# Performance work log

Measured on AMD Instinct MI355X. Metric: run time of the kernel, lower is better.

Reference implementation:

```python
import jax, jax.numpy as jnp
import numpy as np
from math import lgamma

LMAX = 4
SPHERE_FDIM = 512
SO3_F1 = 64
BATCH = 64
IMG = 509
EPS = 1e-5

# ---------- numpy setup-time Wigner / spherical-harmonic machinery ----------

def _lnf(n):
    return lgamma(n + 1.0)

def small_d(l, beta):
    # real Wigner small-d, rows m'=-l..l, cols m=-l..l, beta: (G,)
    G = beta.shape[0]
    d = np.zeros((G, 2*l+1, 2*l+1))
    cb, sb = np.cos(beta/2.0), np.sin(beta/2.0)
    for i, mp in enumerate(range(-l, l+1)):
        for j, m in enumerate(range(-l, l+1)):
            pref = 0.5*(_lnf(l+mp)+_lnf(l-mp)+_lnf(l+m)+_lnf(l-m))
            val = np.zeros(G)
            for k in range(max(0, m-mp), min(l+m, l-mp)+1):
                ln = pref - (_lnf(l+m-k)+_lnf(k)+_lnf(l-mp-k)+_lnf(mp-m+k))
                val += ((-1.0)**(mp-m+k))*np.exp(ln)*cb**(2*l+m-mp-2*k)*sb**(mp-m+2*k)
            d[:, i, j] = val
    return d

def _U(l):
    # complex->real spherical-harmonic change of basis
    U = np.zeros((2*l+1, 2*l+1), dtype=complex)
    U[l, l] = 1.0
    s = 2.0**-0.5
    for m in range(1, l+1):
        U[l+m, l+m] = ((-1)**m)*s
        U[l+m, l-m] = s
        U[l-m, l-m] = 1j*s
        U[l-m, l+m] = -1j*((-1)**m)*s
    return U

def wigner_D(l, a, b, c):
    # real-basis Wigner D, (G, 2l+1, 2l+1)
    d = small_d(l, b)
    m = np.arange(-l, l+1)
    Dc = np.exp(-1j*np.outer(a, m))[:, :, None]*d*np.exp(-1j*np.outer(c, m))[:, None, :]
    U = _U(l)
    return np.real(np.einsum('ij,gjk,lk->gil', U, Dc, U.conj()))

def flat_wigner(lmax, a, b, c):
    # (G, sum_l (2l+1)^2) with sqrt(2l+1) component normalization (orthonormal basis)
    return np.concatenate([np.sqrt(2*l+1.0)*wigner_D(l, a, b, c).reshape(len(a), -1) for l in range(lmax+1)], axis=1)

def sph_harm(lmax, alpha, beta):
    # component-normalized real spherical harmonics, (G, (lmax+1)^2)
    z = np.zeros_like(alpha)
    return np.concatenate([np.sqrt(2*l+1.0)*wigner_D(l, alpha, beta, z)[:, :, l] for l in range(lmax+1)], axis=1)

def fib_sphere(n):
    # quasi-uniform sphere grid (stand-in for healpix grid of same size)
    i = np.arange(n) + 0.5
    beta = np.arccos(1.0 - 2.0*i/n)
    alpha = (np.pi*(1.0+5.0**0.5)*i) % (2.0*np.pi)
    return alpha, beta

def so3_grid(n_s2, n_gamma):
    a, b = fib_sphere(n_s2)
    g = np.linspace(0, 2*np.pi, n_gamma, endpoint=False)
    return np.repeat(a, n_gamma), np.repeat(b, n_gamma), np.tile(g, n_s2)

# ---------- inputs ----------

def setup_inputs() -> dict:
    key = jax.random.key(0)
    ks = jax.random.split(key, 8)
    f32 = jnp.float32
    x = jax.random.normal(ks[0], (BATCH, 1, IMG, IMG), f32)
    conv1_w = jax.random.normal(ks[1], (3, 1, 5, 5), f32)*0.2
    conv1_b = jnp.zeros((3,), f32)
    conv2_w = jax.random.normal(ks[2], (5, 3, 5, 5), f32)*0.12
    conv2_b = jnp.zeros((5,), f32)
    p_w = jax.random.normal(ks[3], (SPHERE_FDIM, 5), f32)*0.4  # projector 1x1 conv
    p_b = jnp.zeros((SPHERE_FDIM,), f32)
    # projector: orthographic-projection gaussian weights onto upper-hemisphere grid
    a_p, b_p = fib_sphere(192)
    msk = b_p <= np.pi/2
    a_p, b_p = a_p[msk], b_p[msk]
    xyz = np.stack([np.sin(b_p)*np.cos(a_p), np.sin(b_p)*np.sin(a_p), np.cos(b_p)], 1)
    max_r = np.max(np.linalg.norm(xyz[:, [0, 2]], axis=1))
    sx, sy = 0.9*xyz[:, 2]/max_r, 0.9*xyz[:, 0]/max_r
    g = np.linspace(-1, 1, 125)
    gx, gy = np.meshgrid(g, g, indexing='ij')
    sig = 0.2
    data = np.exp(-((gx[..., None]-sx)**2 + (gy[..., None]-sy)**2)/(2*sig*sig))/np.sqrt(2*np.pi*sig*sig)
    data = data/data.sum((0, 1), keepdims=True)
    idx = np.arange(20)  # fixed n_subset=20 points (deterministic)
    proj_weight = jnp.asarray(data[:, :, idx], f32)          # (125,125,20) learned param
    Y_proj = jnp.asarray(sph_harm(LMAX, a_p[idx], b_p[idx]), f32)  # (20,25)
    # S2Convolution kernel grid: full sphere, 192 pts
    a_k, b_k = fib_sphere(192)
    Y_s2 = jnp.asarray(sph_harm(LMAX, a_k, b_k), f32)        # (192,25)
    s2_w = jax.random.normal(ks[4], (SPHERE_FDIM, SO3_F1, 192), f32)
    bn_gamma = jnp.ones((165,), f32)
    bn_beta = jnp.zeros((165,), f32)
    # SO3Convolution near-identity kernel grid (8 alpha x 3 beta x 8 gamma)
    beta_k = np.arange(1, 4)*(np.pi/8)/3
    alpha_k = np.linspace(0, 2*np.pi, 8, endpoint=False)
    gamma_k = np.linspace(0, 2*np.pi, 8, endpoint=False)
    A, B, C = np.meshgrid(alpha_k, beta_k, gamma_k, indexing='ij')
    D_so3k = jnp.asarray(flat_wigner(LMAX, A.ravel(), B.ravel(), C.ravel()), f32)  # (192,165)
    so3_w = jax.random.normal(ks[5], (SO3_F1, 1, A.size), f32)
    # SO3Activation grid (576 rotations) and evaluation grid (4608 rotations)
    D_act = jnp.asarray(flat_wigner(LMAX, *so3_grid(48, 12)), f32)             # (576,165)
    eval_wigners = jnp.asarray(flat_wigner(LMAX, *so3_grid(192, 24)).T, f32)   # (165,4608)
    return {"x": x, "conv1_w": conv1_w, "conv1_b": conv1_b, "conv2_w": conv2_w, "conv2_b": conv2_b, "p_w": p_w, "p_b": p_b, "proj_weight": proj_weight, "Y_proj": Y_proj, "s2_w": s2_w, "Y_s2": Y_s2, "bn_gamma": bn_gamma, "bn_beta": bn_beta, "so3_w": so3_w, "D_so3k": D_so3k, "D_act": D_act, "eval_wigners": eval_wigners}

# ---------- forward ----------

def _conv(x, w, b):
    y = jax.lax.conv_general_dilated(x, w, (2, 2), 'VALID', dimension_numbers=('NCHW', 'OIHW', 'NCHW'))
    return y + b[None, :, None, None]

def _forward(x, conv1_w, conv1_b, conv2_w, conv2_b, p_w, p_b, proj_weight, Y_proj, s2_w, Y_s2, bn_gamma, bn_beta, so3_w, D_so3k, D_act, eval_wigners):
    # CNN featurizer: (B,1,509,509) -> (B,5,125,125)
    feat = _conv(jax.nn.relu(_conv(x, conv1_w, conv1_b)), conv2_w, conv2_b)
    f0 = feat[0]  # original forward only uses sample 0
    # Image2Sphere projector: 1x1 conv, gaussian projection to sphere pts, SH expansion
    z = jnp.einsum('chw,oc->ohw', f0, p_w) + p_b[:, None, None]          # (512,125,125)
    pts = jnp.einsum('ohw,hwp->op', z, proj_weight)                       # (512,20)
    harm = jnp.einsum('op,pm->om', pts, Y_proj)/(Y_proj.shape[0]**0.5)    # (512,25)
    psi = jnp.einsum('ni,xyn->xyi', Y_s2, s2_w)/(Y_s2.shape[0]**0.5)      # (512,64,25)
    f_in = harm.shape[0]
    blocks, o = [], 0
    for l in range(LMAX+1):
        d = 2*l+1
        out_l = jnp.einsum('xyu,xm->yum', psi[:, :, o:o+d], harm[:, o:o+d])/(f_in**0.5)
        blocks.append(out_l.reshape(-1, d*d))
        o += d
    h = jnp.concatenate(blocks, axis=1)  # (64,165)
    # SO3Activation: to SO(3) grid, pointwise relu (normalize2mom factor sqrt(2)), back
    s = (2.0**0.5)*jax.nn.relu(jnp.einsum('fi,gi->fg', h, D_act))
    h = jnp.einsum('fg,gi->fi', s, D_act)/D_act.shape[0]
    # BatchNorm1d(165) over the 64-channel 'batch' dim, training statistics
    mu = h.mean(0)
    var = jnp.mean((h - mu)**2, axis=0)
    h = (h - mu)*jax.lax.rsqrt(var + EPS)*bn_gamma + bn_beta
    # SO3Convolution: so3 irreps -> so3 irreps, f_out=1
    psi2 = jnp.einsum('ni,xyn->xyi', D_so3k, so3_w)/(D_so3k.shape[0]**0.5)  # (64,1,165)
    blocks, o = [], 0
    for l in range(LMAX+1):
        d = 2*l+1
        pl = psi2[:, :, o:o+d*d].reshape(SO3_F1, -1, d, d)
        xl = h[:, o:o+d*d].reshape(SO3_F1, d, d)
        out_l = jnp.einsum('xyuv,xvm->yum', pl, xl)/((SO3_F1*d)**0.5)
        blocks.append(out_l.reshape(-1, d*d))
        o += d*d
    harm_out = jnp.concatenate(blocks, axis=1)  # (1,165)
    # probabilities over SO(3) grid: wigner matmul + sigmoid
    return jax.nn.sigmoid(jnp.matmul(harm_out, eval_wigners)).squeeze(0)  # (4608,)

def reference(x, conv1_w, conv1_b, conv2_w, conv2_b, p_w, p_b, proj_weight, Y_proj, s2_w, Y_s2, bn_gamma, bn_beta, so3_w, D_so3k, D_act, eval_wigners):
    return _forward(x, conv1_w, conv1_b, conv2_w, conv2_b, p_w, p_b, proj_weight, Y_proj, s2_w, Y_s2, bn_gamma, bn_beta, so3_w, D_so3k, D_act, eval_wigners)
```

## Files before the change

### kernel.cpp

```cpp
#include <hip/hip_runtime.h>
#include <math.h>

#define IMG 509
#define C1N 253
#define C2N 125
#define NSPH 512
#define NY 64
#define NK 192
#define NH 25
#define NI 165
#define NG 576
#define NE 4608
#define NP 20
#define YN 12288
#define PSPLIT 16

__device__ __forceinline__ void decode_irr(int t, int& l, int& o, int& d, int& u, int& m) {
    if (t < 1)       { l = 0; o = 0;  }
    else if (t < 10) { l = 1; o = 1;  }
    else if (t < 35) { l = 2; o = 10; }
    else if (t < 84) { l = 3; o = 35; }
    else             { l = 4; o = 84; }
    d = 2 * l + 1;
    int r = t - o;
    u = r / d;
    m = r - u * d;
}

__global__ __launch_bounds__(256) void k_conv(const float* __restrict__ x,
        const float* __restrict__ w1, const float* __restrict__ b1,
        const float* __restrict__ w2, const float* __restrict__ b2,
        float* __restrict__ f0) {
    __shared__ float s1[3][35][36];
    __shared__ float sw1[75];
    __shared__ float sw2[375];
    int tid = threadIdx.x;
    if (tid < 75) sw1[tid] = w1[tid];
    for (int j = tid; j < 375; j += 256) sw2[j] = w2[j];
    int OH0 = blockIdx.y * 16, OW0 = blockIdx.x * 16;
    int R0 = 2 * OH0, C0 = 2 * OW0;
    float bb0 = b1[0], bb1 = b1[1], bb2 = b1[2];
    __syncthreads();
    for (int j = tid; j < 35 * 35; j += 256) {
        int rr = j / 35, cc = j - rr * 35;
        int r = R0 + rr, c = C0 + cc;
        float v0 = 0.f, v1 = 0.f, v2 = 0.f;
        if (r < C1N && c < C1N) {
            const float* xp = x + (2 * r) * IMG + 2 * c;
            float a0 = bb0, a1 = bb1, a2 = bb2;
#pragma unroll
            for (int kh = 0; kh < 5; ++kh)
#pragma unroll
                for (int kw = 0; kw < 5; ++kw) {
                    float xv = xp[kh * IMG + kw];
                    a0 = fmaf(xv, sw1[kh * 5 + kw], a0);
                    a1 = fmaf(xv, sw1[25 + kh * 5 + kw], a1);
                    a2 = fmaf(xv, sw1[50 + kh * 5 + kw], a2);
                }
            v0 = fmaxf(a0, 0.f); v1 = fmaxf(a1, 0.f); v2 = fmaxf(a2, 0.f);
        }
        s1[0][rr][cc] = v0; s1[1][rr][cc] = v1; s1[2][rr][cc] = v2;
    }
    __syncthreads();
    int loh = tid >> 4, low = tid & 15;
    int oh = OH0 + loh, ow = OW0 + low;
    if (oh < C2N && ow < C2N) {
        float acc[5] = {b2[0], b2[1], b2[2], b2[3], b2[4]};
#pragma unroll
        for (int ci = 0; ci < 3; ++ci)
#pragma unroll
            for (int kh = 0; kh < 5; ++kh)
#pragma unroll
                for (int kw = 0; kw < 5; ++kw) {
                    float sv = s1[ci][2 * loh + kh][2 * low + kw];
                    int wof = ci * 25 + kh * 5 + kw;
#pragma unroll
                    for (int c = 0; c < 5; ++c)
                        acc[c] = fmaf(sv, sw2[c * 75 + wof], acc[c]);
                }
#pragma unroll
        for (int c = 0; c < 5; ++c)
            f0[c * (C2N * C2N) + oh * C2N + ow] = acc[c];
    }
}

__global__ __launch_bounds__(256) void k_proj(const float* __restrict__ f0,
        const float* __restrict__ proj, float* __restrict__ Gp) {
    int c = blockIdx.x, s = blockIdx.y, tid = threadIdx.x;
    const int HW = C2N * C2N;
    const int CH = (HW + PSPLIT - 1) / PSPLIT;
    int hw_end = min(HW, (s + 1) * CH);
    float acc[NP];
#pragma unroll
    for (int p = 0; p < NP; ++p) acc[p] = 0.0f;
    for (int hw = s * CH + tid; hw < hw_end; hw += 256) {
        float v = (c < 5) ? f0[c * HW + hw] : 1.0f;
        const float* pp = proj + (size_t)hw * NP;
#pragma unroll
        for (int p = 0; p < NP; ++p) acc[p] = fmaf(v, pp[p], acc[p]);
    }
    __shared__ float red[4][NP];
    int lane = tid & 63, wv = tid >> 6;
#pragma unroll
    for (int p = 0; p < NP; ++p) {
        float v = acc[p];
        for (int off = 32; off; off >>= 1) v += __shfl_xor(v, off, 64);
        if (lane == 0) red[wv][p] = v;
    }
    __syncthreads();
    if (tid < NP)
        Gp[(s * 6 + c) * NP + tid] = red[0][tid] + red[1][tid] + red[2][tid] + red[3][tid];
}

__global__ __launch_bounds__(256) void k_harm(const float* __restrict__ Gp,
        const float* __restrict__ p_w, const float* __restrict__ p_b,
        const float* __restrict__ Yp, float* __restrict__ harm) {
    __shared__ float sG[6 * NP];
    __shared__ float sY[NP * NH];
    int tid = threadIdx.x;
    if (tid < 6 * NP) {
        float a = 0.0f;
        for (int s = 0; s < PSPLIT; ++s) a += Gp[s * (6 * NP) + tid];
        sG[tid] = a;
    }
    for (int i = tid; i < NP * NH; i += 256) sY[i] = Yp[i];
    __syncthreads();
    int idx = blockIdx.x * 256 + tid;
    if (idx >= NSPH * NH) return;
    int o = idx / NH, m = idx - o * NH;
    float pb = p_b[o];
    const float* pw = p_w + o * 5;
    float acc = 0.0f;
#pragma unroll
    for (int p = 0; p < NP; ++p) {
        float pts = pb * sG[5 * NP + p];
#pragma unroll
        for (int cc = 0; cc < 5; ++cc) pts = fmaf(pw[cc], sG[cc * NP + p], pts);
        acc = fmaf(pts, sY[p * NH + m], acc);
    }
    harm[idx] = acc * (1.0f / 4.47213595499957939f);
}

#define XCH 64
__global__ __launch_bounds__(256) void k_T(const float* __restrict__ s2w,
        const float* __restrict__ harm, float* __restrict__ T, int atomic) {
    int yn = blockIdx.x * 256 + threadIdx.x;
    int x0 = blockIdx.y * XCH;
    __shared__ float sh[XCH * NH];
    for (int i = threadIdx.x; i < XCH * NH; i += 256) sh[i] = harm[x0 * NH + i];
    __syncthreads();
    float acc[NH];
#pragma unroll
    for (int m = 0; m < NH; ++m) acc[m] = 0.0f;
    const float* ap = s2w + (size_t)x0 * YN + yn;
#pragma unroll 8
    for (int xi = 0; xi < XCH; ++xi) {
        float a = ap[(size_t)xi * YN];
        const float* hr = sh + xi * NH;
#pragma unroll
        for (int m = 0; m < NH; ++m) acc[m] = fmaf(a, hr[m], acc[m]);
    }
    if (atomic) {
#pragma unroll
        for (int m = 0; m < NH; ++m) atomicAdd(T + (size_t)m * YN + yn, acc[m]);
    } else {
        float* tp = T + (size_t)(blockIdx.y * NH) * YN + yn;
#pragma unroll
        for (int m = 0; m < NH; ++m) tp[(size_t)m * YN] = acc[m];
    }
}

__global__ __launch_bounds__(576) void k_so3block(const float* __restrict__ T,
        const float* __restrict__ Ys2, const float* __restrict__ Dact,
        float* __restrict__ h2, int nparts) {
    int y = blockIdx.x, tid = threadIdx.x;
    __shared__ float sY[NK * NH];
    __shared__ float sT[NK * NH];
    __shared__ float shh[NI];
    __shared__ float ss[NG];
    for (int i = tid; i < NK * NH; i += NG) sY[i] = Ys2[i];
    for (int j = tid; j < NK * NH; j += NG) {
        int m = j / NK, n = j - m * NK;
        float acc = 0.0f;
        const float* tp = T + (size_t)m * YN + y * NK + n;
        for (int p = 0; p < nparts; ++p) acc += tp[(size_t)p * NH * YN];
        sT[n * NH + m] = acc;
    }
    __syncthreads();
    if (tid < NI) {
        int l, o, d, u, m;
        decode_irr(tid, l, o, d, u, m);
        int cu = l * l + u, cm = l * l + m;
        float acc = 0.0f;
        for (int n = 0; n < NK; ++n)
            acc = fmaf(sY[n * NH + cu], sT[n * NH + cm], acc);
        shh[tid] = acc * (1.0f / 313.534098402587976f);
    }
    __syncthreads();
    {
        const float* dr = Dact + (size_t)tid * NI;
        float acc = 0.0f;
        for (int i = 0; i < NI; ++i) acc = fmaf(shh[i], dr[i], acc);
        ss[tid] = 1.41421356237309515f * fmaxf(acc, 0.0f);
    }
    __syncthreads();
    if (tid < NI) {
        float acc = 0.0f;
        for (int g = 0; g < NG; ++g) acc = fmaf(ss[g], Dact[(size_t)g * NI + tid], acc);
        h2[y * NI + tid] = acc * (1.0f / (float)NG);
    }
}

__global__ __launch_bounds__(192) void k_psi2(const float* __restrict__ w,
        const float* __restrict__ D, float* __restrict__ psi2) {
    __shared__ float sw[NK];
    int x = blockIdx.x, t = threadIdx.x;
    if (t < NK) sw[t] = w[x * NK + t];
    __syncthreads();
    if (t >= NI) return;
    float acc = 0.0f;
    for (int n = 0; n < NK; ++n) acc = fmaf(sw[n], D[(size_t)n * NI + t], acc);
    psi2[x * NI + t] = acc * (1.0f / 13.8564064605510175f);
}

__global__ __launch_bounds__(192) void k_eval(const float* __restrict__ psi2,
        const float* __restrict__ h2, const float* __restrict__ gamma,
        const float* __restrict__ beta, const float* __restrict__ ew,
        float* __restrict__ out) {
    __shared__ float sp[NY * NI];
    __shared__ float sh[NY * NI];
    __shared__ float sho[NI];
    int tid = threadIdx.x;
    for (int i = tid; i < NY * NI; i += 192) { sp[i] = psi2[i]; sh[i] = h2[i]; }
    __syncthreads();
    if (tid < NI) {
        float s = 0.0f;
        for (int f = 0; f < NY; ++f) s += sh[f * NI + tid];
        float mu = s * (1.0f / NY);
        float v = 0.0f;
        for (int f = 0; f < NY; ++f) { float d = sh[f * NI + tid] - mu; v = fmaf(d, d, v); }
        float sc = rsqrtf(v * (1.0f / NY) + 1e-5f) * gamma[tid];
        float bt = beta[tid];
        for (int f = 0; f < NY; ++f) sh[f * NI + tid] = (sh[f * NI + tid] - mu) * sc + bt;
    }
    __syncthreads();
    if (tid < NI) {
        int l, o, d, u, m;
        decode_irr(tid, l, o, d, u, m);
        const float invsc[5] = {0.125f, 0.0721687836487032f, 0.0559016994374947f,
                                0.0472455591261534f, 0.0416666666666667f};
        float acc = 0.0f;
        for (int x = 0; x < NY; ++x) {
            const float* pr = sp + x * NI + o;
            const float* hr = sh + x * NI + o;
            for (int v = 0; v < d; ++v) acc = fmaf(pr[u * d + v], hr[v * d + m], acc);
        }
        sho[tid] = acc * invsc[l];
    }
    __syncthreads();
    if (tid < 96) {
        int g = blockIdx.x * 96 + tid;
        float acc = 0.0f;
        for (int i = 0; i < NI; ++i) acc = fmaf(sho[i], ew[(size_t)i * NE + g], acc);
        out[g] = 1.0f / (1.0f + expf(-acc));
    }
}

extern "C" void kernel_launch(void* const* d_in, const int* in_sizes, int n_in,
                              void* d_out, int out_size, void* d_ws, size_t ws_size,
                              hipStream_t stream) {
    const float* x      = (const float*)d_in[0];
    const float* c1w    = (const float*)d_in[1];
    const float* c1b    = (const float*)d_in[2];
    const float* c2w    = (const float*)d_in[3];
    const float* c2b    = (const float*)d_in[4];
    const float* p_w    = (const float*)d_in[5];
    const float* p_b    = (const float*)d_in[6];
    const float* projw  = (const float*)d_in[7];
    const float* Yp     = (const float*)d_in[8];
    const float* s2w    = (const float*)d_in[9];
    const float* Ys2    = (const float*)d_in[10];
    const float* gamma  = (const float*)d_in[11];
    const float* beta   = (const float*)d_in[12];
    const float* so3w   = (const float*)d_in[13];
    const float* Dso3k  = (const float*)d_in[14];
    const float* Dact   = (const float*)d_in[15];
    const float* ew     = (const float*)d_in[16];
    float* out = (float*)d_out;

    float* ws   = (float*)d_ws;
    float* f0   = ws;
    float* Gp   = f0 + 78128;
    float* harm = Gp + 1920;
    float* h2   = harm + 12800;
    float* psi2 = h2 + 10560;
    float* T    = psi2 + 10560;

    const size_t base = 78128 + 1920 + 12800 + 10560 + 10560;
    bool big = ws_size >= (base + 8u * 307200u) * sizeof(float);
    int nparts = big ? 8 : 1;
    if (!big) hipMemsetAsync(T, 0, (size_t)307200 * sizeof(float), stream);

    k_conv<<<dim3(8, 8), 256, 0, stream>>>(x, c1w, c1b, c2w, c2b, f0);
    k_proj<<<dim3(6, PSPLIT), 256, 0, stream>>>(f0, projw, Gp);
    k_harm<<<(NSPH * NH + 255) / 256, 256, 0, stream>>>(Gp, p_w, p_b, Yp, harm);
    k_T<<<dim3(48, 8), 256, 0, stream>>>(s2w, harm, T, big ? 0 : 1);
    k_so3block<<<NY, NG, 0, stream>>>(T, Ys2, Dact, h2, nparts);
    k_psi2<<<NY, 192, 0, stream>>>(so3w, Dso3k, psi2);
    k_eval<<<48, 192, 0, stream>>>(psi2, h2, gamma, beta, ew, out);
}
```

Baseline: 249.6 us.

## Fuse conv, projection, transpose and psi2 into one prologue kernel; refactor T stage

Merges the conv, projection, psi2, the T zeroing and a new Dact transpose into a single multi-role prologue kernel, so the pipeline runs as four launches instead of seven plus a memset. The conv is recomputed per output channel in row strips and fused directly with the projection reduction. The T stage now folds p_w/p_b in algebraically, accumulating 6 coefficients per s2w element instead of 25, and always uses atomics into a single T buffer. The final kernel splits the wigner dot over 4 wave-groups with 64 outputs per block, and so3block reads a transposed Dact for coalesced access. In exchange, the conv is redone once per output channel, and the T stage now always pays atomic contention where it previously could write per-part buffers when the workspace was large.

```diff
diff --git a/kernel.cpp b/kernel.cpp
--- a/kernel.cpp
+++ b/kernel.cpp
@@ -13,7 +13,6 @@
 #define NE 4608
 #define NP 20
 #define YN 12288
-#define PSPLIT 16
 
 __device__ __forceinline__ void decode_irr(int t, int& l, int& o, int& d, int& u, int& m) {
     if (t < 1)       { l = 0; o = 0;  }
@@ -27,152 +26,158 @@
     m = r - u * d;
 }
 
-__global__ __launch_bounds__(256) void k_conv(const float* __restrict__ x,
+__global__ __launch_bounds__(256) void k_pre(const float* __restrict__ x,
         const float* __restrict__ w1, const float* __restrict__ b1,
         const float* __restrict__ w2, const float* __restrict__ b2,
-        float* __restrict__ f0) {
-    __shared__ float s1[3][35][36];
+        const float* __restrict__ projw,
+        const float* __restrict__ Dact, float* __restrict__ DactT,
+        const float* __restrict__ so3w, const float* __restrict__ Dso3k,
+        float* __restrict__ psi2, float* __restrict__ Gp, float* __restrict__ T) {
+    __shared__ float s1[3 * 13 * 254];
     __shared__ float sw1[75];
-    __shared__ float sw2[375];
+    __shared__ float sw2[75];
+    __shared__ float red[4][NP];
+    int b = blockIdx.x, tid = threadIdx.x;
+    if (b < 150) {
+        int c = b / 25, s = b - 25 * c;
+        float acc[NP];
+#pragma unroll
+        for (int p = 0; p < NP; ++p) acc[p] = 0.0f;
+        if (c < 5) {
+            if (tid < 75) { sw1[tid] = w1[tid]; sw2[tid] = w2[c * 75 + tid]; }
+            __syncthreads();
+            float bb0 = b1[0], bb1 = b1[1], bb2 = b1[2];
+            for (int j = tid; j < 13 * 253; j += 256) {
+                int lq = j / 253, col = j - lq * 253;
+                int q = 10 * s + lq;
+                const float* xp = x + (2 * q) * IMG + 2 * col;
+                float a0 = bb0, a1 = bb1, a2 = bb2;
+#pragma unroll
+                for (int kh = 0; kh < 5; ++kh)
+#pragma unroll
+                    for (int kw = 0; kw < 5; ++kw) {
+                        float xv = xp[kh * IMG + kw];
+                        a0 = fmaf(xv, sw1[kh * 5 + kw], a0);
+                        a1 = fmaf(xv, sw1[25 + kh * 5 + kw], a1);
+                        a2 = fmaf(xv, sw1[50 + kh * 5 + kw], a2);
+                    }
+                s1[lq * 254 + col] = fmaxf(a0, 0.f);
+                s1[13 * 254 + lq * 254 + col] = fmaxf(a1, 0.f);
+                s1[2 * 13 * 254 + lq * 254 + col] = fmaxf(a2, 0.f);
+            }
+            __syncthreads();
+            float b2c = b2[c];
+            for (int j = tid; j < 625; j += 256) {
+                int lr = j / 125, ow = j - lr * 125;
+                float v = b2c;
+#pragma unroll
+                for (int ci = 0; ci < 3; ++ci)
+#pragma unroll
+                    for (int kh = 0; kh < 5; ++kh)
+#pragma unroll
+                        for (int kw = 0; kw < 5; ++kw)
+                            v = fmaf(s1[ci * (13 * 254) + (2 * lr + kh) * 254 + 2 * ow + kw],
+                                     sw2[ci * 25 + kh * 5 + kw], v);
+                const float* pp = projw + (size_t)(625 * s + j) * NP;
+#pragma unroll
+                for (int p = 0; p < NP; ++p) acc[p] = fmaf(v, pp[p], acc[p]);
+            }
+        } else {
+            for (int j = tid; j < 625; j += 256) {
+                const float* pp = projw + (size_t)(625 * s + j) * NP;
+#pragma unroll
+                for (int p = 0; p < NP; ++p) acc[p] += pp[p];
+            }
+        }
+        int lane = tid & 63, wv = tid >> 6;
+#pragma unroll
+        for (int p = 0; p < NP; ++p) {
+            float v = acc[p];
+            for (int off = 32; off; off >>= 1) v += __shfl_xor(v, off, 64);
+            if (lane == 0) red[wv][p] = v;
+        }
+        __syncthreads();
+        if (tid < NP)
+            Gp[(s * 6 + c) * NP + tid] = red[0][tid] + red[1][tid] + red[2][tid] + red[3][tid];
+    } else if (b < 522) {
+        int j = (b - 150) * 256 + tid;
+        if (j < NG * NI) {
+            int g = j / NI, i = j - g * NI;
+            DactT[(size_t)i * NG + g] = Dact[j];
+        }
+    } else if (b < 586) {
+        __shared__ float sw[NK];
+        int xx = b - 522;
+        if (tid < NK) sw[tid] = so3w[xx * NK + tid];
+        __syncthreads();
+        if (tid < NI) {
+            float a = 0.0f;
+            for (int n = 0; n < NK; ++n) a = fmaf(sw[n], Dso3k[(size_t)n * NI + tid], a);
+            psi2[xx * NI + tid] = a * (1.0f / 13.8564064605510175f);
+        }
+    } else {
+        int j = ((b - 586) * 256 + tid) * 4;
+        if (j < NH * YN) {
+            float4 z = {0.f, 0.f, 0.f, 0.f};
+            *(float4*)(T + j) = z;
+        }
+    }
+}
+
+__global__ __launch_bounds__(256) void k_T2(const float* __restrict__ s2w,
+        const float* __restrict__ Gp, const float* __restrict__ Yp,
+        const float* __restrict__ p_w, const float* __restrict__ p_b,
+        float* __restrict__ T) {
+    __shared__ float sG[120];
+    __shared__ float sM[150];
+    __shared__ float spw[320];
+    __shared__ float spb[64];
     int tid = threadIdx.x;
-    if (tid < 75) sw1[tid] = w1[tid];
-    for (int j = tid; j < 375; j += 256) sw2[j] = w2[j];
-    int OH0 = blockIdx.y * 16, OW0 = blockIdx.x * 16;
-    int R0 = 2 * OH0, C0 = 2 * OW0;
-    float bb0 = b1[0], bb1 = b1[1], bb2 = b1[2];
-    __syncthreads();
-    for (int j = tid; j < 35 * 35; j += 256) {
-        int rr = j / 35, cc = j - rr * 35;
-        int r = R0 + rr, c = C0 + cc;
-        float v0 = 0.f, v1 = 0.f, v2 = 0.f;
-        if (r < C1N && c < C1N) {
-            const float* xp = x + (2 * r) * IMG + 2 * c;
-            float a0 = bb0, a1 = bb1, a2 = bb2;
-#pragma unroll
-            for (int kh = 0; kh < 5; ++kh)
-#pragma unroll
-                for (int kw = 0; kw < 5; ++kw) {
-                    float xv = xp[kh * IMG + kw];
-                    a0 = fmaf(xv, sw1[kh * 5 + kw], a0);
-                    a1 = fmaf(xv, sw1[25 + kh * 5 + kw], a1);
-                    a2 = fmaf(xv, sw1[50 + kh * 5 + kw], a2);
-                }
-            v0 = fmaxf(a0, 0.f); v1 = fmaxf(a1, 0.f); v2 = fmaxf(a2, 0.f);
-        }
-        s1[0][rr][cc] = v0; s1[1][rr][cc] = v1; s1[2][rr][cc] = v2;
-    }
-    __syncthreads();
-    int loh = tid >> 4, low = tid & 15;
-    int oh = OH0 + loh, ow = OW0 + low;
-    if (oh < C2N && ow < C2N) {
-        float acc[5] = {b2[0], b2[1], b2[2], b2[3], b2[4]};
-#pragma unroll
-        for (int ci = 0; ci < 3; ++ci)
-#pragma unroll
-            for (int kh = 0; kh < 5; ++kh)
-#pragma unroll
-                for (int kw = 0; kw < 5; ++kw) {
-                    float sv = s1[ci][2 * loh + kh][2 * low + kw];
-                    int wof = ci * 25 + kh * 5 + kw;
-#pragma unroll
-                    for (int c = 0; c < 5; ++c)
-                        acc[c] = fmaf(sv, sw2[c * 75 + wof], acc[c]);
-                }
-#pragma unroll
-        for (int c = 0; c < 5; ++c)
-            f0[c * (C2N * C2N) + oh * C2N + ow] = acc[c];
-    }
-}
-
-__global__ __launch_bounds__(256) void k_proj(const float* __restrict__ f0,
-        const float* __restrict__ proj, float* __restrict__ Gp) {
-    int c = blockIdx.x, s = blockIdx.y, tid = threadIdx.x;
-    const int HW = C2N * C2N;
-    const int CH = (HW + PSPLIT - 1) / PSPLIT;
-    int hw_end = min(HW, (s + 1) * CH);
-    float acc[NP];
-#pragma unroll
-    for (int p = 0; p < NP; ++p) acc[p] = 0.0f;
-    for (int hw = s * CH + tid; hw < hw_end; hw += 256) {
-        float v = (c < 5) ? f0[c * HW + hw] : 1.0f;
-        const float* pp = proj + (size_t)hw * NP;
-#pragma unroll
-        for (int p = 0; p < NP; ++p) acc[p] = fmaf(v, pp[p], acc[p]);
-    }
-    __shared__ float red[4][NP];
-    int lane = tid & 63, wv = tid >> 6;
-#pragma unroll
-    for (int p = 0; p < NP; ++p) {
-        float v = acc[p];
-        for (int off = 32; off; off >>= 1) v += __shfl_xor(v, off, 64);
-        if (lane == 0) red[wv][p] = v;
-    }
-    __syncthreads();
-    if (tid < NP)
-        Gp[(s * 6 + c) * NP + tid] = red[0][tid] + red[1][tid] + red[2][tid] + red[3][tid];
-}
-
-__global__ __launch_bounds__(256) void k_harm(const float* __restrict__ Gp,
-        const float* __restrict__ p_w, const float* __restrict__ p_b,
-        const float* __restrict__ Yp, float* __restrict__ harm) {
-    __shared__ float sG[6 * NP];
-    __shared__ float sY[NP * NH];
-    int tid = threadIdx.x;
-    if (tid < 6 * NP) {
+    if (tid < 120) {
         float a = 0.0f;
-        for (int s = 0; s < PSPLIT; ++s) a += Gp[s * (6 * NP) + tid];
+        for (int s = 0; s < 25; ++s) a += Gp[s * 120 + tid];
         sG[tid] = a;
     }
-    for (int i = tid; i < NP * NH; i += 256) sY[i] = Yp[i];
-    __syncthreads();
-    int idx = blockIdx.x * 256 + tid;
-    if (idx >= NSPH * NH) return;
-    int o = idx / NH, m = idx - o * NH;
-    float pb = p_b[o];
-    const float* pw = p_w + o * 5;
-    float acc = 0.0f;
-#pragma unroll
-    for (int p = 0; p < NP; ++p) {
-        float pts = pb * sG[5 * NP + p];
-#pragma unroll
-        for (int cc = 0; cc < 5; ++cc) pts = fmaf(pw[cc], sG[cc * NP + p], pts);
-        acc = fmaf(pts, sY[p * NH + m], acc);
-    }
-    harm[idx] = acc * (1.0f / 4.47213595499957939f);
-}
-
-#define XCH 64
-__global__ __launch_bounds__(256) void k_T(const float* __restrict__ s2w,
-        const float* __restrict__ harm, float* __restrict__ T, int atomic) {
-    int yn = blockIdx.x * 256 + threadIdx.x;
-    int x0 = blockIdx.y * XCH;
-    __shared__ float sh[XCH * NH];
-    for (int i = threadIdx.x; i < XCH * NH; i += 256) sh[i] = harm[x0 * NH + i];
-    __syncthreads();
-    float acc[NH];
-#pragma unroll
-    for (int m = 0; m < NH; ++m) acc[m] = 0.0f;
+    int x0 = blockIdx.y * 64;
+    for (int i = tid; i < 320; i += 256) spw[i] = p_w[x0 * 5 + i];
+    if (tid < 64) spb[tid] = p_b[x0 + tid];
+    __syncthreads();
+    if (tid < 150) {
+        int c = tid / 25, m = tid - 25 * c;
+        float a = 0.0f;
+#pragma unroll
+        for (int p = 0; p < NP; ++p) a = fmaf(sG[c * NP + p], Yp[p * NH + m], a);
+        sM[tid] = a * 0.22360679774997896f;
+    }
+    __syncthreads();
+    int yn = blockIdx.x * 256 + tid;
+    float w0 = 0.f, w1v = 0.f, w2v = 0.f, w3 = 0.f, w4 = 0.f, wb = 0.f;
     const float* ap = s2w + (size_t)x0 * YN + yn;
 #pragma unroll 8
-    for (int xi = 0; xi < XCH; ++xi) {
+    for (int xi = 0; xi < 64; ++xi) {
         float a = ap[(size_t)xi * YN];
-        const float* hr = sh + xi * NH;
-#pragma unroll
-        for (int m = 0; m < NH; ++m) acc[m] = fmaf(a, hr[m], acc[m]);
-    }
-    if (atomic) {
-#pragma unroll
-        for (int m = 0; m < NH; ++m) atomicAdd(T + (size_t)m * YN + yn, acc[m]);
-    } else {
-        float* tp = T + (size_t)(blockIdx.y * NH) * YN + yn;
-#pragma unroll
-        for (int m = 0; m < NH; ++m) tp[(size_t)m * YN] = acc[m];
+        w0 = fmaf(a, spw[xi * 5 + 0], w0);
+        w1v = fmaf(a, spw[xi * 5 + 1], w1v);
+        w2v = fmaf(a, spw[xi * 5 + 2], w2v);
+        w3 = fmaf(a, spw[xi * 5 + 3], w3);
+        w4 = fmaf(a, spw[xi * 5 + 4], w4);
+        wb = fmaf(a, spb[xi], wb);
+    }
+#pragma unroll
+    for (int m = 0; m < NH; ++m) {
+        float v = wb * sM[125 + m];
+        v = fmaf(w0, sM[m], v);
+        v = fmaf(w1v, sM[25 + m], v);
+        v = fmaf(w2v, sM[50 + m], v);
+        v = fmaf(w3, sM[75 + m], v);
+        v = fmaf(w4, sM[100 + m], v);
+        atomicAdd(T + (size_t)m * YN + yn, v);
     }
 }
 
 __global__ __launch_bounds__(576) void k_so3block(const float* __restrict__ T,
         const float* __restrict__ Ys2, const float* __restrict__ Dact,
-        float* __restrict__ h2, int nparts) {
+        const float* __restrict__ DactT, float* __restrict__ h2) {
     int y = blockIdx.x, tid = threadIdx.x;
     __shared__ float sY[NK * NH];
     __shared__ float sT[NK * NH];
@@ -181,10 +186,7 @@
     for (int i = tid; i < NK * NH; i += NG) sY[i] = Ys2[i];
     for (int j = tid; j < NK * NH; j += NG) {
         int m = j / NK, n = j - m * NK;
-        float acc = 0.0f;
-        const float* tp = T + (size_t)m * YN + y * NK + n;
-        for (int p = 0; p < nparts; ++p) acc += tp[(size_t)p * NH * YN];
-        sT[n * NH + m] = acc;
+        sT[n * NH + m] = T[(size_t)m * YN + y * NK + n];
     }
     __syncthreads();
     if (tid < NI) {
@@ -198,9 +200,9 @@
     }
     __syncthreads();
     {
-        const float* dr = Dact + (size_t)tid * NI;
-        float acc = 0.0f;
-        for (int i = 0; i < NI; ++i) acc = fmaf(shh[i], dr[i], acc);
+        float acc = 0.0f;
+        for (int i = 0; i < NI; ++i)
+            acc = fmaf(shh[i], DactT[(size_t)i * NG + tid], acc);
         ss[tid] = 1.41421356237309515f * fmaxf(acc, 0.0f);
     }
     __syncthreads();
@@ -211,27 +213,16 @@
     }
 }
 
-__global__ __launch_bounds__(192) void k_psi2(const float* __restrict__ w,
-        const float* __restrict__ D, float* __restrict__ psi2) {
-    __shared__ float sw[NK];
-    int x = blockIdx.x, t = threadIdx.x;
-    if (t < NK) sw[t] = w[x * NK + t];
-    __syncthreads();
-    if (t >= NI) return;
-    float acc = 0.0f;
-    for (int n = 0; n < NK; ++n) acc = fmaf(sw[n], D[(size_t)n * NI + t], acc);
-    psi2[x * NI + t] = acc * (1.0f / 13.8564064605510175f);
-}
-
-__global__ __launch_bounds__(192) void k_eval(const float* __restrict__ psi2,
+__global__ __launch_bounds__(256) void k_final(const float* __restrict__ psi2,
         const float* __restrict__ h2, const float* __restrict__ gamma,
         const float* __restrict__ beta, const float* __restrict__ ew,
         float* __restrict__ out) {
     __shared__ float sp[NY * NI];
     __shared__ float sh[NY * NI];
     __shared__ float sho[NI];
+    __shared__ float sred[256];
     int tid = threadIdx.x;
-    for (int i = tid; i < NY * NI; i += 192) { sp[i] = psi2[i]; sh[i] = h2[i]; }
+    for (int i = tid; i < NY * NI; i += 256) { sp[i] = psi2[i]; sh[i] = h2[i]; }
     __syncthreads();
     if (tid < NI) {
         float s = 0.0f;
@@ -250,19 +241,24 @@
         const float invsc[5] = {0.125f, 0.0721687836487032f, 0.0559016994374947f,
                                 0.0472455591261534f, 0.0416666666666667f};
         float acc = 0.0f;
-        for (int x = 0; x < NY; ++x) {
-            const float* pr = sp + x * NI + o;
-            const float* hr = sh + x * NI + o;
-            for (int v = 0; v < d; ++v) acc = fmaf(pr[u * d + v], hr[v * d + m], acc);
+        for (int xx = 0; xx < NY; ++xx) {
+            const float* pr = sp + xx * NI + o + u * d;
+            const float* hr = sh + xx * NI + o + m;
+            for (int v = 0; v < d; ++v) acc = fmaf(pr[v], hr[v * d], acc);
         }
         sho[tid] = acc * invsc[l];
     }
     __syncthreads();
-    if (tid < 96) {
-        int g = blockIdx.x * 96 + tid;
-        float acc = 0.0f;
-        for (int i = 0; i < NI; ++i) acc = fmaf(sho[i], ew[(size_t)i * NE + g], acc);
-        out[g] = 1.0f / (1.0f + expf(-acc));
+    int iq = tid >> 6, gl = tid & 63;
+    int g = blockIdx.x * 64 + gl;
+    int i0 = iq * 42, i1 = min(NI, i0 + 42);
+    float a = 0.0f;
+    for (int i = i0; i < i1; ++i) a = fmaf(sho[i], ew[(size_t)i * NE + g], a);
+    sred[tid] = a;
+    __syncthreads();
+    if (tid < 64) {
+        float v = sred[tid] + sred[64 + tid] + sred[128 + tid] + sred[192 + tid];
+        out[blockIdx.x * 64 + tid] = 1.0f / (1.0f + expf(-v));
     }
 }
 
@@ -288,24 +284,16 @@
     const float* ew     = (const float*)d_in[16];
     float* out = (float*)d_out;
 
-    float* ws   = (float*)d_ws;
-    float* f0   = ws;
-    float* Gp   = f0 + 78128;
-    float* harm = Gp + 1920;
-    float* h2   = harm + 12800;
-    float* psi2 = h2 + 10560;
-    float* T    = psi2 + 10560;
-
-    const size_t base = 78128 + 1920 + 12800 + 10560 + 10560;
-    bool big = ws_size >= (base + 8u * 307200u) * sizeof(float);
-    int nparts = big ? 8 : 1;
-    if (!big) hipMemsetAsync(T, 0, (size_t)307200 * sizeof(float), stream);
-
-    k_conv<<<dim3(8, 8), 256, 0, stream>>>(x, c1w, c1b, c2w, c2b, f0);
-    k_proj<<<dim3(6, PSPLIT), 256, 0, stream>>>(f0, projw, Gp);
-    k_harm<<<(NSPH * NH + 255) / 256, 256, 0, stream>>>(Gp, p_w, p_b, Yp, harm);
-    k_T<<<dim3(48, 8), 256, 0, stream>>>(s2w, harm, T, big ? 0 : 1);
-    k_so3block<<<NY, NG, 0, stream>>>(T, Ys2, Dact, h2, nparts);
-    k_psi2<<<NY, 192, 0, stream>>>(so3w, Dso3k, psi2);
-    k_eval<<<48, 192, 0, stream>>>(psi2, h2, gamma, beta, ew, out);
-}
+    float* ws    = (float*)d_ws;
+    float* Gp    = ws;
+    float* psi2  = Gp + 3008;
+    float* h2    = psi2 + 10560;
+    float* DactT = h2 + 10560;
+    float* T     = DactT + 95040;
+
+    k_pre<<<886, 256, 0, stream>>>(x, c1w, c1b, c2w, c2b, projw, Dact, DactT,
+                                   so3w, Dso3k, psi2, Gp, T);
+    k_T2<<<dim3(48, 8), 256, 0, stream>>>(s2w, Gp, Yp, p_w, p_b, T);
+    k_so3block<<<NY, NG, 0, stream>>>(T, Ys2, Dact, DactT, h2);
+    k_final<<<72, 256, 0, stream>>>(psi2, h2, gamma, beta, ew, out);
+}
```

Result: faster. 225.9 us (-9.5%).
